# Performance work log

Hardware: AMD Instinct MI355X
Metric: run time of the kernel (lower is better)

Reference implementation:

```python
import math
import jax, jax.numpy as jnp
import numpy as np
from jax import lax

B, C, O, K, WDIM, H, W = 8, 512, 512, 3, 512, 64, 64
CONV_SCALE = 1.0 / math.sqrt(C * K * K)
MOD_SCALE = 1.0 / math.sqrt(WDIM)


def setup_inputs() -> dict:
    key = jax.random.key(0)
    k1, k2, k3, k4 = jax.random.split(key, 4)
    return {
        "x": jax.random.normal(k1, (B, C, H, W), dtype=jnp.float32),
        "w": jax.random.normal(k2, (B, WDIM), dtype=jnp.float32),
        "base_weight": jax.random.normal(k3, (1, O, C, K, K), dtype=jnp.float32),
        "mod_weight": jax.random.normal(k4, (C, WDIM), dtype=jnp.float32),
        "mod_bias": jnp.zeros((C,), dtype=jnp.float32),
    }


def reference(x, w, base_weight, mod_weight, mod_bias):
    # EqualLinear modulation: s in (B, C), then +1
    s = w @ (mod_weight * MOD_SCALE).T + mod_bias + 1.0  # (B, C)
    # Per-sample modulated weights: (B, O, C, K, K)
    weight = CONV_SCALE * base_weight * s[:, None, :, None, None]
    # Demodulation
    d = lax.rsqrt(jnp.sum(weight * weight, axis=(2, 3, 4), keepdims=True))
    weight = weight * d
    pad = K // 2

    def conv_one(xi, wi):
        # xi: (C, H, W), wi: (O, C, K, K)
        return lax.conv_general_dilated(
            xi[None], wi, window_strides=(1, 1),
            padding=[(pad, pad), (pad, pad)],
            dimension_numbers=("NCHW", "OIHW", "NCHW"),
        )[0]

    return jax.vmap(conv_one)(x, weight)  # (B, O, H, W)
```

## Files before the change

kernel.cpp:

```cpp
#include <hip/hip_runtime.h>
#include <stdint.h>


#define MOD_SCALE  0.044194173824159216f
#define CONV_SCALE 0.014731391274719739f

typedef __attribute__((ext_vector_type(4))) float f32x4;
typedef __attribute__((ext_vector_type(8))) short bf16x8;

__device__ inline unsigned short f2bf(float f) {
  uint32_t u = __float_as_uint(f);
  uint32_t r = (u + 0x7fffu + ((u >> 16) & 1u)) >> 16;
  return (unsigned short)r;
}

__device__ inline void gload_lds16(const void* g, void* l) {
  __builtin_amdgcn_global_load_lds(
      (const __attribute__((address_space(1))) void*)g,
      (__attribute__((address_space(3))) void*)l, 16, 0, 0);
}

__global__ __launch_bounds__(256) void k_style(const float* __restrict__ w,
                                               const float* __restrict__ modw,
                                               const float* __restrict__ modb,
                                               float* __restrict__ s_out) {
  __shared__ float red[256];
  const int tid = threadIdx.x;
  const int sb = blockIdx.x;
  const int cb = sb & 7, b = sb >> 3;
  const int cl = tid >> 2, qq = tid & 3;
  const int c = (cb << 6) + cl;
  const float4* wd = (const float4*)(w + (b << 9) + (qq << 7));
  const float4* md = (const float4*)(modw + ((size_t)c << 9) + (qq << 7));
  float acc = 0.f;
#pragma unroll
  for (int i = 0; i < 32; ++i) {
    float4 a = wd[i], m = md[i];
    acc += a.x * m.x + a.y * m.y + a.z * m.z + a.w * m.w;
  }
  red[tid] = acc;
  __syncthreads();
  if (tid < 64) {
    float v = red[tid * 4] + red[tid * 4 + 1] + red[tid * 4 + 2] + red[tid * 4 + 3];
    int cc = (cb << 6) + tid;
    s_out[(b << 9) + cc] = v * MOD_SCALE + modb[cc] + 1.0f;
  }
}

__global__ __launch_bounds__(256) void k_mid(const float* __restrict__ bw,
                                             const float* __restrict__ s,
                                             unsigned short* __restrict__ awT,
                                             float* __restrict__ d_out,
                                             const float* __restrict__ x,
                                             unsigned short* __restrict__ xp) {
  __shared__ uint32_t tb[64 * 260];
  const int blk = blockIdx.x;
  const int tid = threadIdx.x;

  if (blk < 512) {
    float* lw  = (float*)tb;
    float* ls  = lw + 4608;
    float* red = ls + 4096;
    const int o = blk;
    {
      const float4* src = (const float4*)(bw + (size_t)o * 4608);
      float4* dst = (float4*)lw;
#pragma unroll
      for (int i = 0; i < 4; ++i) dst[tid + (i << 8)] = src[tid + (i << 8)];
      if (tid < 128) dst[tid + 1024] = src[tid + 1024];
    }
    {
      const float4* src = (const float4*)s;
      float4* dst = (float4*)ls;
#pragma unroll
      for (int i = 0; i < 4; ++i) dst[tid + (i << 8)] = src[tid + (i << 8)];
    }
    __syncthreads();
    const int c0 = tid << 1;
    const int base = c0 * 9;
    float wq0 = 0.f, wq1 = 0.f;
#pragma unroll
    for (int j = 0; j < 9; ++j) {
      float a = lw[base + j];      wq0 += a * a;
      float b2 = lw[base + 9 + j]; wq1 += b2 * b2;
    }
    const int lane = tid & 63, wv = tid >> 6;
#pragma unroll
    for (int b = 0; b < 8; ++b) {
      float s0 = ls[(b << 9) + c0], s1 = ls[(b << 9) + c0 + 1];
      float v = wq0 * s0 * s0 + wq1 * s1 * s1;
#pragma unroll
      for (int off = 32; off > 0; off >>= 1) v += __shfl_down(v, off, 64);
      if (lane == 0) red[(b << 2) + wv] = v;
    }
    __syncthreads();
    if (tid < 8) {
      float a = red[tid << 2] + red[(tid << 2) + 1] + red[(tid << 2) + 2] + red[(tid << 2) + 3];
      d_out[(tid << 9) + o] = rsqrtf(a * (1.0f / 4608.0f)) * CONV_SCALE;
    }
    uint32_t* dst = (uint32_t*)(awT + (size_t)o * 4608);
#pragma unroll
    for (int j = 0; j < 9; ++j)
      dst[(j << 8) + tid] = (uint32_t)f2bf(lw[base + j]) |
                            ((uint32_t)f2bf(lw[base + 9 + j]) << 16);
  } else if (blk < 1024) {
    const int q = blk - 512;
    const int b = q >> 6, y = q & 63;
    const int px4 = tid & 15;
    const int cp  = tid >> 4;
    const float* xb = x + (size_t)(b << 9) * 4096 + (y << 6) + (px4 << 2);
    const float* sb = s + (b << 9);
#pragma unroll
    for (int it = 0; it < 16; ++it) {
      const int cpair = cp + (it << 4);
      const int c0 = cpair << 1;
      const float4 a0 = *(const float4*)(xb + (size_t)c0 * 4096);
      const float4 a1 = *(const float4*)(xb + (size_t)(c0 + 1) * 4096);
      const float s0 = sb[c0], s1 = sb[c0 + 1];
      const int pxb = px4 << 2;
      tb[(pxb + 0) * 260 + cpair] = (uint32_t)f2bf(a0.x * s0) | ((uint32_t)f2bf(a1.x * s1) << 16);
      tb[(pxb + 1) * 260 + cpair] = (uint32_t)f2bf(a0.y * s0) | ((uint32_t)f2bf(a1.y * s1) << 16);
      tb[(pxb + 2) * 260 + cpair] = (uint32_t)f2bf(a0.z * s0) | ((uint32_t)f2bf(a1.z * s1) << 16);
      tb[(pxb + 3) * 260 + cpair] = (uint32_t)f2bf(a0.w * s0) | ((uint32_t)f2bf(a1.w * s1) << 16);
    }
    __syncthreads();
    const int wv = tid >> 6, l = tid & 63;
    uint32_t* xpw = (uint32_t*)xp;
#pragma unroll
    for (int it = 0; it < 16; ++it) {
      const int px = (wv << 4) + it;
      const uint4 v = *(const uint4*)(tb + px * 260 + (l << 2));
      const size_t base = ((size_t)b * 4356 + (size_t)(y + 1) * 66 + (px + 1)) << 8;
      ((uint4*)(xpw + base))[l] = v;
    }
  } else {
    const int q = blk - 1024;
    const int b = q / 260, p = q - b * 260;
    int py, px;
    if (p < 66)       { py = 0;       px = p; }
    else if (p < 132) { py = 65;      px = p - 66; }
    else if (p < 196) { py = p - 131; px = 0; }
    else              { py = p - 195; px = 65; }
    uint32_t* dst = (uint32_t*)(xp + ((size_t)b * 4356 + py * 66 + px) * 512);
    dst[tid] = 0u;
  }
}

__global__ __launch_bounds__(512, 1) void k_conv(const unsigned short* __restrict__ awT,
                                                 const unsigned short* __restrict__ xpad,
                                                 const float* __restrict__ dmod,
                                                 float* __restrict__ out) {
  __shared__ alignas(16) unsigned short As[2][16384];
  __shared__ alignas(16) unsigned short Bs[2][16896];
  const int tid = threadIdx.x;

  const int nI = blockIdx.x;
  const int m0 = blockIdx.y << 8;
  const int b  = blockIdx.z;
  const int n0 = nI << 8;
  const int y0 = nI << 2;

  const int srow = tid >> 3;
  const int schk = ((tid & 7) - (srow & 7)) & 7;
  const int scol = schk << 3;

  const unsigned short* A0 = awT + (size_t)(m0 + srow) * 4608 + scol;
  const size_t bx = (size_t)b * (66 * 66 * 512);
  const unsigned short* B0 = xpad + bx + (size_t)(y0 * 66 + srow) * 512 + scol;

  const int lane = tid & 63;
  const int wv   = tid >> 6;
  const int moff = (wv >> 1) << 6;
  const int lm   = lane & 15;
  const int g4   = lane >> 4;

  const int arow = moff + lm;
  int aoff[2];
#pragma unroll
  for (int h = 0; h < 2; ++h)
    aoff[h] = arow * 64 + ((((h << 2) + g4) + arow) & 7) * 8;
  int boff[3][2][2];
#pragma unroll
  for (int kx = 0; kx < 3; ++kx)
#pragma unroll
    for (int jr = 0; jr < 2; ++jr) {
      const int rb = ((wv & 1) * 2 + jr) * 66 + lm + kx;
#pragma unroll
      for (int h = 0; h < 2; ++h)
        boff[kx][jr][h] = rb * 64 + ((((h << 2) + g4) + rb) & 7) * 8;
    }

  f32x4 acc[4][8];
#pragma unroll
  for (int i = 0; i < 4; ++i)
#pragma unroll
    for (int j = 0; j < 8; ++j) acc[i][j] = (f32x4){0.f, 0.f, 0.f, 0.f};

  auto stageA = [&](int buf, int ky, int kx, int kb) {
    const unsigned short* Ap = A0 + (((ky * 3 + kx) << 9) + (kb << 6));
#pragma unroll
    for (int g = 0; g < 4; ++g)
      gload_lds16(Ap + (size_t)(g << 6) * 4608, &As[buf][(g << 12) + (tid << 3)]);
  };
  auto stageB = [&](int buf, int ky, int kb) {
    const unsigned short* Bp = B0 + (size_t)(ky * 66) * 512 + (kb << 6);
#pragma unroll
    for (int g = 0; g < 4; ++g)
      gload_lds16(Bp + (size_t)(g << 6) * 512, &Bs[buf][(g << 12) + (tid << 3)]);
    if (tid < 64) gload_lds16(Bp + (size_t)256 * 512, &Bs[buf][16384 + (tid << 3)]);
  };
  auto mstep = [&](int ab, int bb, int kx) {
    __builtin_amdgcn_s_setprio(1);
#pragma unroll
    for (int h = 0; h < 2; ++h) {
      bf16x8 af[4], bfr[8];
      const unsigned short* pa = As[ab] + aoff[h];
#pragma unroll
      for (int i = 0; i < 4; ++i) af[i] = *(const bf16x8*)(pa + (i << 10));
#pragma unroll
      for (int j = 0; j < 8; ++j)
        bfr[j] = *(const bf16x8*)(Bs[bb] + boff[kx][j >> 2][h] + ((j & 3) << 10));
#pragma unroll
      for (int i = 0; i < 4; ++i)
#pragma unroll
        for (int j = 0; j < 8; ++j)
          acc[i][j] = __builtin_amdgcn_mfma_f32_16x16x32_bf16(af[i], bfr[j], acc[i][j], 0, 0, 0);
    }
    __builtin_amdgcn_s_setprio(0);
  };

  stageA(0, 0, 0, 0);
  stageB(0, 0, 0);
  __syncthreads();

  int ab = 0, bb = 0;
#pragma unroll 1
  for (int ky = 0; ky < 3; ++ky) {
#pragma unroll 1
    for (int kb = 0; kb < 8; ++kb) {
      stageA(ab ^ 1, ky, 1, kb);
      mstep(ab, bb, 0);
      __syncthreads();
      ab ^= 1;
      stageA(ab ^ 1, ky, 2, kb);
      mstep(ab, bb, 1);
      __syncthreads();
      ab ^= 1;
      const int nky = (kb == 7) ? ky + 1 : ky;
      const int nkb = (kb == 7) ? 0 : kb + 1;
      if (!(ky == 2 && kb == 7)) {
        stageA(ab ^ 1, nky, 0, nkb);
        stageB(bb ^ 1, nky, nkb);
      }
      mstep(ab, bb, 2);
      __syncthreads();
      ab ^= 1;
      bb ^= 1;
    }
  }

  const float* dB = dmod + (b << 9) + m0 + moff;
  float* op = out + (size_t)((b << 9) + m0 + moff) * 4096 + n0 + ((wv & 1) << 7);
#pragma unroll
  for (int i = 0; i < 4; ++i) {
#pragma unroll
    for (int r = 0; r < 4; ++r) {
      const int m = i * 16 + (g4 << 2) + r;
      const float dm = dB[m];
#pragma unroll
      for (int j = 0; j < 8; ++j)
        op[(size_t)m * 4096 + (j << 4) + lm] = acc[i][j][r] * dm;
    }
  }
}

extern "C" void kernel_launch(void* const* d_in, const int* in_sizes, int n_in,
                              void* d_out, int out_size, void* d_ws, size_t ws_size,
                              hipStream_t stream) {
  const float* x    = (const float*)d_in[0];
  const float* w    = (const float*)d_in[1];
  const float* bw   = (const float*)d_in[2];
  const float* modw = (const float*)d_in[3];
  const float* modb = (const float*)d_in[4];
  float* out = (float*)d_out;
  char* ws = (char*)d_ws;

  float* s_buf = (float*)(ws);
  float* d_buf = (float*)(ws + 16384);
  unsigned short* awT  = (unsigned short*)(ws + 32768);
  unsigned short* xpad = (unsigned short*)(ws + 4751360);

  (void)in_sizes; (void)n_in; (void)out_size; (void)ws_size;

  k_style<<<64,   256, 0, stream>>>(w, modw, modb, s_buf);
  k_mid  <<<3104, 256, 0, stream>>>(bw, s_buf, awT, d_buf, x, xpad);
  k_conv <<<dim3(16, 2, 8), 512, 0, stream>>>(awT, xpad, d_buf, out);
}
```

Baseline: 265.1 us.

## Prefetch two stages ahead with explicit vmcnt waits instead of syncthreads

Reworks the implicit-GEMM conv main loop so A tiles are issued one extra stage ahead, and each mstep waits on partial vmcnt counts with raw s_barrier instead of a full __syncthreads drain. The B tail load is spread across all waves (8 lanes each) instead of only wave 0, so every wave has the same number of outstanding loads for the vmcnt counting. This is meant to keep more global-to-LDS loads in flight while MFMAs run. It relies on hand-counted vmcnt values and on barriers placed to guard LDS buffer reuse, which is fragile.

```diff
diff --git a/kernel.cpp b/kernel.cpp
--- a/kernel.cpp
+++ b/kernel.cpp
@@ -207,7 +207,12 @@
 #pragma unroll
     for (int g = 0; g < 4; ++g)
       gload_lds16(Bp + (size_t)(g << 6) * 512, &Bs[buf][(g << 12) + (tid << 3)]);
-    if (tid < 64) gload_lds16(Bp + (size_t)256 * 512, &Bs[buf][16384 + (tid << 3)]);
+    if (lane < 8) {
+      const int rchk = (lane - wv) & 7;
+      const unsigned short* gp = xpad + bx +
+          (size_t)((y0 + ky) * 66 + 256 + wv) * 512 + (rchk << 3) + (kb << 6);
+      gload_lds16(gp, &Bs[buf][16384 + (wv << 6) + (lane << 3)]);
+    }
   };
   auto mstep = [&](int ab, int bb, int kx) {
     __builtin_amdgcn_s_setprio(1);
@@ -231,32 +236,37 @@
 
   stageA(0, 0, 0, 0);
   stageB(0, 0, 0);
-  __syncthreads();
+  stageA(1, 0, 1, 0);
 
   int ab = 0, bb = 0;
 #pragma unroll 1
-  for (int ky = 0; ky < 3; ++ky) {
-#pragma unroll 1
-    for (int kb = 0; kb < 8; ++kb) {
-      stageA(ab ^ 1, ky, 1, kb);
-      mstep(ab, bb, 0);
-      __syncthreads();
-      ab ^= 1;
-      stageA(ab ^ 1, ky, 2, kb);
-      mstep(ab, bb, 1);
-      __syncthreads();
-      ab ^= 1;
-      const int nky = (kb == 7) ? ky + 1 : ky;
-      const int nkb = (kb == 7) ? 0 : kb + 1;
-      if (!(ky == 2 && kb == 7)) {
-        stageA(ab ^ 1, nky, 0, nkb);
-        stageB(bb ^ 1, nky, nkb);
-      }
-      mstep(ab, bb, 2);
-      __syncthreads();
-      ab ^= 1;
-      bb ^= 1;
-    }
+  for (int t = 0; t < 24; ++t) {
+    const int ky = t >> 3, kb = t & 7;
+    const int nky = (kb == 7) ? ky + 1 : ky;
+    const int nkb = (kb == 7) ? 0 : kb + 1;
+    asm volatile("s_waitcnt vmcnt(4)" ::: "memory");
+    __builtin_amdgcn_sched_barrier(0);
+    __builtin_amdgcn_s_barrier();
+    mstep(ab, bb, 0);
+    __builtin_amdgcn_s_barrier();
+    stageA(ab, ky, 2, kb);
+    ab ^= 1;
+    asm volatile("s_waitcnt vmcnt(4)" ::: "memory");
+    __builtin_amdgcn_sched_barrier(0);
+    __builtin_amdgcn_s_barrier();
+    mstep(ab, bb, 1);
+    __builtin_amdgcn_s_barrier();
+    if (t < 23) { stageA(ab, nky, 0, nkb); stageB(bb ^ 1, nky, nkb); }
+    ab ^= 1;
+    if (t < 23) asm volatile("s_waitcnt vmcnt(9)" ::: "memory");
+    else        asm volatile("s_waitcnt vmcnt(0)" ::: "memory");
+    __builtin_amdgcn_sched_barrier(0);
+    __builtin_amdgcn_s_barrier();
+    mstep(ab, bb, 2);
+    __builtin_amdgcn_s_barrier();
+    if (t < 23) stageA(ab, nky, 1, nkb);
+    ab ^= 1;
+    bb ^= 1;
   }
 
   const float* dB = dmod + (b << 9) + m0 + moff;
```

New measurement: 267.5 us. Within noise of the previous version (+0.9%).
